# Performance work log

Measured on AMD Instinct MI355X. Metric: run time of the kernel, lower is better.

Reference implementation:

```python
import jax, jax.numpy as jnp
import numpy as np
from jax import lax

NUM_CLASSES = 80
SCALE_XY = 1.0
NMS_THRESH = 0.7
SCORE_THRESH = 0.05
OBJ_THRESH = 0.5
MAX_DETS = 100  # fixed top-K candidate pool fed to NMS (jit-friendly padding)


def setup_inputs() -> dict:
    key = jax.random.key(0)
    k1, k2 = jax.random.split(key)
    x = jax.random.normal(k1, (16, 255, 128, 128), dtype=jnp.float32)
    anchors = jax.random.uniform(k2, (3, 2), dtype=jnp.float32, minval=0.05, maxval=0.7)
    return {"x": x, "anchors": anchors}


def decode(x, anchors):
    # x: [b, A*(5+C), h, w] -> boxes [b,h,w,A,4], obj [b,h,w,A], scores [b,h,w,A,C]
    b, _, h, w = x.shape
    A = anchors.shape[0]
    out = x.reshape(b, A, 5 + NUM_CLASSES, h, w).transpose(0, 3, 4, 1, 2)
    c_x = jnp.arange(w, dtype=jnp.float32).reshape(1, 1, w, 1)
    c_y = jnp.arange(h, dtype=jnp.float32).reshape(1, h, 1, 1)
    b_xy = SCALE_XY * jax.nn.sigmoid(out[..., :2]) - 0.5 * (SCALE_XY - 1.0)
    b_x = (b_xy[..., 0] + c_x) / w
    b_y = (b_xy[..., 1] + c_y) / h
    b_wh = jnp.clip(jnp.exp(out[..., 2:4]) * anchors.reshape(1, 1, 1, A, 2), 0.0, 2.0)
    top_left = jnp.stack([b_x, b_y], axis=-1) - 0.5 * b_wh
    boxes = jnp.concatenate([top_left, top_left + b_wh], axis=-1)
    return boxes, out[..., 4], out[..., 5:]


def box_iou(a, b):
    # a: [N,4], b: [M,4] in (x1,y1,x2,y2)
    area_a = jnp.clip(a[:, 2] - a[:, 0], 0) * jnp.clip(a[:, 3] - a[:, 1], 0)
    area_b = jnp.clip(b[:, 2] - b[:, 0], 0) * jnp.clip(b[:, 3] - b[:, 1], 0)
    lt = jnp.maximum(a[:, None, :2], b[None, :, :2])
    rb = jnp.minimum(a[:, None, 2:], b[None, :, 2:])
    wh = jnp.clip(rb - lt, 0)
    inter = wh[..., 0] * wh[..., 1]
    union = area_a[:, None] + area_b[None, :] - inter
    return inter / jnp.maximum(union, 1e-12)


def greedy_nms(iou, valid):
    # boxes assumed sorted by descending score; valid: [K] bool
    K = iou.shape[0]
    idx = jnp.arange(K)

    def body(i, keep):
        # if box i is kept, suppress later boxes overlapping it too much
        sup = keep[i] & (iou[i] > NMS_THRESH) & (idx > i)
        return keep & ~sup

    return lax.fori_loop(0, K, body, valid)


def _per_image(boxes, b_o, b_scores):
    # boxes [h,w,A,4], b_o [h,w,A], b_scores [h,w,A,C]
    boxes = jnp.clip(boxes.reshape(-1, 4), 0.0, 1.0)
    obj = jax.nn.sigmoid(b_o.reshape(-1))
    cls = jax.nn.sigmoid(b_scores.reshape(-1, NUM_CLASSES))
    cls_score = cls.max(axis=-1)
    labels = jnp.argmax(cls, axis=-1)
    scores = cls_score * obj
    valid = (obj >= OBJ_THRESH) & (scores >= SCORE_THRESH)
    masked = jnp.where(valid, scores, -1.0)
    top_s, top_i = lax.top_k(masked, MAX_DETS)
    top_boxes = boxes[top_i]
    top_labels = labels[top_i]
    cand = top_s > 0.0
    keep = greedy_nms(box_iou(top_boxes, top_boxes), cand)
    out_boxes = jnp.where(keep[:, None], top_boxes, 0.0)
    out_scores = jnp.where(keep, top_s, 0.0)
    out_labels = jnp.where(keep, top_labels, -1)
    return out_boxes, out_scores, out_labels, keep


def reference(x, anchors):
    boxes, b_o, b_scores = decode(x, anchors)
    # fixed-size padded detections per image (equivalent to post_process with
    # dynamic lists, padded to MAX_DETS; keep mask marks valid rows)
    return jax.vmap(_per_image)(boxes, b_o, b_scores)
```

## Files before the change

### kernel.cpp

```cpp
#include <hip/hip_runtime.h>
#include <math.h>

#define B 16
#define A 3
#define W 128
#define HW 16384
#define NCH 255
#define NCLS 80
#define NCAND 49152
#define K 100
#define NBINS 4096
#define CAP 1024

__device__ __forceinline__ float sigmoidf_(float v) {
    return 1.0f / (1.0f + expf(-v));
}

__device__ __forceinline__ bool pair_before(float sa, int ia, float sb, int ib) {
    return (sa > sb) || (sa == sb && ia < ib);
}

__global__ __launch_bounds__(256) void k_scores(const float* __restrict__ x,
                                                float* __restrict__ scores,
                                                unsigned char* __restrict__ labels) {
    int tid = blockIdx.x * 256 + threadIdx.x;
    int g = tid & 3;
    int grp = tid >> 2;
    int b = grp / (A * HW / 4);
    int r = grp - b * (A * HW / 4);
    int a = r / (HW / 4);
    int q = r - a * (HW / 4);
    int hw = q * 4;
    const float* base = x + (size_t)(b * NCH + a * 85) * HW + hw;

    float4 o4 = make_float4(0.f, 0.f, 0.f, 0.f);
    if (g == 0) o4 = *(const float4*)(base + 4 * HW);

    int c0 = g * 20;
    float4 m4 = *(const float4*)(base + (size_t)(5 + c0) * HW);
    int amx = c0, amy = c0, amz = c0, amw = c0;
    #pragma unroll
    for (int k = 1; k < 20; ++k) {
        int c = c0 + k;
        float4 v = *(const float4*)(base + (size_t)(5 + c) * HW);
        bool gx = v.x > m4.x; amx = gx ? c : amx; m4.x = gx ? v.x : m4.x;
        bool gy = v.y > m4.y; amy = gy ? c : amy; m4.y = gy ? v.y : m4.y;
        bool gz = v.z > m4.z; amz = gz ? c : amz; m4.z = gz ? v.z : m4.z;
        bool gw = v.w > m4.w; amw = gw ? c : amw; m4.w = gw ? v.w : m4.w;
    }
    #pragma unroll
    for (int d = 1; d <= 2; d <<= 1) {
        float vx = __shfl_xor(m4.x, d); int jx = __shfl_xor(amx, d);
        float vy = __shfl_xor(m4.y, d); int jy = __shfl_xor(amy, d);
        float vz = __shfl_xor(m4.z, d); int jz = __shfl_xor(amz, d);
        float vw = __shfl_xor(m4.w, d); int jw = __shfl_xor(amw, d);
        if (vx > m4.x || (vx == m4.x && jx < amx)) { m4.x = vx; amx = jx; }
        if (vy > m4.y || (vy == m4.y && jy < amy)) { m4.y = vy; amy = jy; }
        if (vz > m4.z || (vz == m4.z && jz < amz)) { m4.z = vz; amz = jz; }
        if (vw > m4.w || (vw == m4.w && jw < amw)) { m4.w = vw; amw = jw; }
    }

    if (g == 0) {
        float ol[4] = {o4.x, o4.y, o4.z, o4.w};
        float ml[4] = {m4.x, m4.y, m4.z, m4.w};
        float outv[4];
        #pragma unroll
        for (int l = 0; l < 4; ++l) {
            float obj = sigmoidf_(ol[l]);
            float cls = sigmoidf_(ml[l]);
            float sc = obj * cls;
            bool valid = (obj >= 0.5f) && (sc >= 0.05f);
            outv[l] = valid ? sc : -1.0f;
        }
        size_t off = (size_t)b * NCAND + a * HW + hw;
        *(float4*)(scores + off) = make_float4(outv[0], outv[1], outv[2], outv[3]);
        *(uchar4*)(labels + off) = make_uchar4((unsigned char)amx, (unsigned char)amy,
                                               (unsigned char)amz, (unsigned char)amw);
    }
}

__global__ __launch_bounds__(1024) void k_tail(const float* __restrict__ x,
                                               const float* __restrict__ anchors,
                                               const float* __restrict__ scores,
                                               const unsigned char* __restrict__ labels,
                                               float* __restrict__ out) {
    __shared__ unsigned int lh[NBINS];
    __shared__ int sh_thr;
    __shared__ unsigned int sh_cnt;
    __shared__ float cs[CAP];
    __shared__ int ci[CAP];
    __shared__ float ts[K];
    __shared__ int tix[K];
    __shared__ float bx[K][4];
    __shared__ float area[K];
    __shared__ int lab[K];
    __shared__ unsigned int sup[K][4];
    __shared__ unsigned int keepw[4];

    int b = blockIdx.x;
    int tid = threadIdx.x;
    const float* sb = scores + (size_t)b * NCAND;

    for (int i = tid; i < NBINS; i += 1024) lh[i] = 0;
    if (tid == 0) { sh_thr = 0; sh_cnt = 0; }
    if (tid < 4) keepw[tid] = 0u;
    for (int i = tid; i < K * 4; i += 1024) ((unsigned int*)sup)[i] = 0u;
    if (tid < K) { ts[tid] = -3.0f; tix[tid] = 0x7FFFFFFF; }
    __syncthreads();

    #pragma unroll
    for (int it = 0; it < 12; ++it) {
        int o = (it * 1024 + tid) * 4;
        float4 v = *(const float4*)(sb + o);
        float sv[4] = {v.x, v.y, v.z, v.w};
        #pragma unroll
        for (int l = 0; l < 4; ++l) {
            float s = sv[l];
            if (s > 0.0f) {
                int bin = (int)(s * (float)NBINS);
                bin = bin > NBINS - 1 ? NBINS - 1 : bin;
                atomicAdd(&lh[bin], 1u);
            }
        }
    }
    __syncthreads();

    if (tid < 64) {
        unsigned int c = 0;
        #pragma unroll
        for (int j = 0; j < 64; ++j)
            c += lh[tid * 64 + ((j + tid) & 63)];
        unsigned int s = c;
        #pragma unroll
        for (int off = 1; off < 64; off <<= 1) {
            unsigned int v = __shfl_down(s, off);
            if (tid + off < 64) s += v;
        }
        unsigned long long mask = __ballot(s >= K);
        int lstar = -1;
        if (mask) lstar = 63 - __clzll(mask);
        unsigned int snext = 0;
        if (lstar >= 0 && lstar < 63) snext = (unsigned int)__shfl((int)s, lstar + 1);
        if (lstar >= 0 && tid == lstar) {
            unsigned int running = snext;
            int result = lstar * 64;
            for (int bin = lstar * 64 + 63; bin >= lstar * 64; --bin) {
                running += lh[bin];
                if (running >= K) { result = bin; break; }
            }
            sh_thr = result;
        }
    }
    __syncthreads();

    int thr = sh_thr;
    #pragma unroll
    for (int it = 0; it < 12; ++it) {
        int o = (it * 1024 + tid) * 4;
        float4 v = *(const float4*)(sb + o);
        float sv[4] = {v.x, v.y, v.z, v.w};
        #pragma unroll
        for (int l = 0; l < 4; ++l) {
            float s = sv[l];
            if (s > 0.0f && (int)(s * (float)NBINS) >= thr) {
                unsigned int p = atomicAdd(&sh_cnt, 1u);
                if (p < CAP) {
                    int so = o + l;
                    int aa = so >> 14;
                    int hh = so & (HW - 1);
                    cs[p] = s;
                    ci[p] = hh * A + aa;
                }
            }
        }
    }
    __syncthreads();
    int n = (int)sh_cnt; if (n > CAP) n = CAP;

    if (tid < n) {
        float s0 = cs[tid]; int i0 = ci[tid];
        int rank = 0;
        for (int j = 0; j < n; ++j)
            rank += pair_before(cs[j], ci[j], s0, i0) ? 1 : 0;
        if (rank < K) { ts[rank] = s0; tix[rank] = i0; }
    }
    __syncthreads();

    if (tid < K && ts[tid] > 0.0f) {
        int nidx = tix[tid];
        int a = nidx % A;
        int hw = nidx / A;
        int cx = hw % W;
        int cy = hw / W;
        const float* base = x + (size_t)(b * NCH + a * 85) * HW + hw;
        float tx = base[0];
        float ty = base[HW];
        float tw = base[2 * HW];
        float th = base[3 * HW];
        float bcx = (sigmoidf_(tx) + (float)cx) / 128.0f;
        float bcy = (sigmoidf_(ty) + (float)cy) / 128.0f;
        float bw = fminf(fmaxf(expf(tw) * anchors[a * 2 + 0], 0.0f), 2.0f);
        float bh = fminf(fmaxf(expf(th) * anchors[a * 2 + 1], 0.0f), 2.0f);
        float x1 = bcx - 0.5f * bw;
        float y1 = bcy - 0.5f * bh;
        float x2 = x1 + bw;
        float y2 = y1 + bh;
        x1 = fminf(fmaxf(x1, 0.0f), 1.0f);
        y1 = fminf(fmaxf(y1, 0.0f), 1.0f);
        x2 = fminf(fmaxf(x2, 0.0f), 1.0f);
        y2 = fminf(fmaxf(y2, 0.0f), 1.0f);
        bx[tid][0] = x1; bx[tid][1] = y1; bx[tid][2] = x2; bx[tid][3] = y2;
        area[tid] = fmaxf(x2 - x1, 0.0f) * fmaxf(y2 - y1, 0.0f);
        lab[tid] = (int)labels[(size_t)b * NCAND + a * HW + hw];
        atomicOr(&keepw[tid >> 5], 1u << (tid & 31));
    }
    __syncthreads();

    for (int p = tid; p < K * K; p += 1024) {
        int i = p / K, j = p % K;
        if (j > i && ts[i] > 0.0f && ts[j] > 0.0f) {
            float lx = fmaxf(bx[i][0], bx[j][0]);
            float ly = fmaxf(bx[i][1], bx[j][1]);
            float rx = fminf(bx[i][2], bx[j][2]);
            float ry = fminf(bx[i][3], bx[j][3]);
            float iw = fmaxf(rx - lx, 0.0f);
            float ih = fmaxf(ry - ly, 0.0f);
            float inter = iw * ih;
            float uni = area[i] + area[j] - inter;
            float iou = inter / fmaxf(uni, 1e-12f);
            if (iou > 0.7f) atomicOr(&sup[i][j >> 5], 1u << (j & 31));
        }
    }
    __syncthreads();

    if (tid == 0) {
        unsigned int kw0 = keepw[0], kw1 = keepw[1], kw2 = keepw[2], kw3 = keepw[3];
        for (int i = 0; i < K; ++i) {
            unsigned int kwi = (i < 32) ? kw0 : (i < 64) ? kw1 : (i < 96) ? kw2 : kw3;
            if ((kwi >> (i & 31)) & 1u) {
                kw0 &= ~sup[i][0];
                kw1 &= ~sup[i][1];
                kw2 &= ~sup[i][2];
                kw3 &= ~sup[i][3];
            }
        }
        keepw[0] = kw0; keepw[1] = kw1; keepw[2] = kw2; keepw[3] = kw3;
    }
    __syncthreads();

    if (tid < K) {
        int kp = (keepw[tid >> 5] >> (tid & 31)) & 1u;
        float sc = ts[tid];
        float* ob = out + (size_t)b * K * 4;
        float* osc = out + (size_t)B * K * 4;
        float* olab = osc + (size_t)B * K;
        float* okp = olab + (size_t)B * K;
        ob[tid * 4 + 0] = kp ? bx[tid][0] : 0.0f;
        ob[tid * 4 + 1] = kp ? bx[tid][1] : 0.0f;
        ob[tid * 4 + 2] = kp ? bx[tid][2] : 0.0f;
        ob[tid * 4 + 3] = kp ? bx[tid][3] : 0.0f;
        osc[b * K + tid] = kp ? sc : 0.0f;
        olab[b * K + tid] = kp ? (float)lab[tid] : -1.0f;
        okp[b * K + tid] = kp ? 1.0f : 0.0f;
    }
}

extern "C" void kernel_launch(void* const* d_in, const int* in_sizes, int n_in,
                              void* d_out, int out_size, void* d_ws, size_t ws_size,
                              hipStream_t stream) {
    const float* x = (const float*)d_in[0];
    const float* anchors = (const float*)d_in[1];
    float* out = (float*)d_out;

    float* scores = (float*)d_ws;
    unsigned char* labels = (unsigned char*)(scores + (size_t)B * NCAND);

    k_scores<<<(B * A * HW) / 256, 256, 0, stream>>>(x, scores, labels);
    k_tail<<<B, 1024, 0, stream>>>(x, anchors, scores, labels, out);
}
```

Baseline: 72.94 us.

## Fuse score pass and per-image tail into one kernel via last-block counter

Merges the class max/argmax scoring kernel and the per-image top-K/NMS tail into one kernel. Each image gets 12 blocks of 1024 threads, and each thread now scans all 80 classes for 4 pixels instead of splitting the classes over 4 threads. A per-image atomic counter, zeroed by a small extra kernel, lets the last finishing block run the selection and NMS. This removes the dependency gap between the two launches. In exchange the grid shrinks to 192 blocks with fewer threads per pixel, which may cut the loads in flight on a bandwidth-bound read.

```diff
diff --git a/kernel.cpp b/kernel.cpp
--- a/kernel.cpp
+++ b/kernel.cpp
@@ -11,6 +11,7 @@
 #define K 100
 #define NBINS 4096
 #define CAP 1024
+#define BLKS_PER_IMG 12
 
 __device__ __forceinline__ float sigmoidf_(float v) {
     return 1.0f / (1.0f + expf(-v));
@@ -20,70 +21,16 @@
     return (sa > sb) || (sa == sb && ia < ib);
 }
 
-__global__ __launch_bounds__(256) void k_scores(const float* __restrict__ x,
-                                                float* __restrict__ scores,
-                                                unsigned char* __restrict__ labels) {
-    int tid = blockIdx.x * 256 + threadIdx.x;
-    int g = tid & 3;
-    int grp = tid >> 2;
-    int b = grp / (A * HW / 4);
-    int r = grp - b * (A * HW / 4);
-    int a = r / (HW / 4);
-    int q = r - a * (HW / 4);
-    int hw = q * 4;
-    const float* base = x + (size_t)(b * NCH + a * 85) * HW + hw;
-
-    float4 o4 = make_float4(0.f, 0.f, 0.f, 0.f);
-    if (g == 0) o4 = *(const float4*)(base + 4 * HW);
-
-    int c0 = g * 20;
-    float4 m4 = *(const float4*)(base + (size_t)(5 + c0) * HW);
-    int amx = c0, amy = c0, amz = c0, amw = c0;
-    #pragma unroll
-    for (int k = 1; k < 20; ++k) {
-        int c = c0 + k;
-        float4 v = *(const float4*)(base + (size_t)(5 + c) * HW);
-        bool gx = v.x > m4.x; amx = gx ? c : amx; m4.x = gx ? v.x : m4.x;
-        bool gy = v.y > m4.y; amy = gy ? c : amy; m4.y = gy ? v.y : m4.y;
-        bool gz = v.z > m4.z; amz = gz ? c : amz; m4.z = gz ? v.z : m4.z;
-        bool gw = v.w > m4.w; amw = gw ? c : amw; m4.w = gw ? v.w : m4.w;
-    }
-    #pragma unroll
-    for (int d = 1; d <= 2; d <<= 1) {
-        float vx = __shfl_xor(m4.x, d); int jx = __shfl_xor(amx, d);
-        float vy = __shfl_xor(m4.y, d); int jy = __shfl_xor(amy, d);
-        float vz = __shfl_xor(m4.z, d); int jz = __shfl_xor(amz, d);
-        float vw = __shfl_xor(m4.w, d); int jw = __shfl_xor(amw, d);
-        if (vx > m4.x || (vx == m4.x && jx < amx)) { m4.x = vx; amx = jx; }
-        if (vy > m4.y || (vy == m4.y && jy < amy)) { m4.y = vy; amy = jy; }
-        if (vz > m4.z || (vz == m4.z && jz < amz)) { m4.z = vz; amz = jz; }
-        if (vw > m4.w || (vw == m4.w && jw < amw)) { m4.w = vw; amw = jw; }
-    }
-
-    if (g == 0) {
-        float ol[4] = {o4.x, o4.y, o4.z, o4.w};
-        float ml[4] = {m4.x, m4.y, m4.z, m4.w};
-        float outv[4];
-        #pragma unroll
-        for (int l = 0; l < 4; ++l) {
-            float obj = sigmoidf_(ol[l]);
-            float cls = sigmoidf_(ml[l]);
-            float sc = obj * cls;
-            bool valid = (obj >= 0.5f) && (sc >= 0.05f);
-            outv[l] = valid ? sc : -1.0f;
-        }
-        size_t off = (size_t)b * NCAND + a * HW + hw;
-        *(float4*)(scores + off) = make_float4(outv[0], outv[1], outv[2], outv[3]);
-        *(uchar4*)(labels + off) = make_uchar4((unsigned char)amx, (unsigned char)amy,
-                                               (unsigned char)amz, (unsigned char)amw);
-    }
-}
-
-__global__ __launch_bounds__(1024) void k_tail(const float* __restrict__ x,
-                                               const float* __restrict__ anchors,
-                                               const float* __restrict__ scores,
-                                               const unsigned char* __restrict__ labels,
-                                               float* __restrict__ out) {
+__global__ __launch_bounds__(64) void k_zero(unsigned int* __restrict__ done) {
+    if (threadIdx.x < B) done[threadIdx.x] = 0u;
+}
+
+__global__ __launch_bounds__(1024, 8) void k_fused(const float* __restrict__ x,
+                                                   const float* __restrict__ anchors,
+                                                   float* __restrict__ scores,
+                                                   unsigned char* __restrict__ labels,
+                                                   unsigned int* __restrict__ done,
+                                                   float* __restrict__ out) {
     __shared__ unsigned int lh[NBINS];
     __shared__ int sh_thr;
     __shared__ unsigned int sh_cnt;
@@ -91,14 +38,62 @@
     __shared__ int ci[CAP];
     __shared__ float ts[K];
     __shared__ int tix[K];
-    __shared__ float bx[K][4];
+    __shared__ float bxs[K][4];
     __shared__ float area[K];
     __shared__ int lab[K];
     __shared__ unsigned int sup[K][4];
     __shared__ unsigned int keepw[4];
-
-    int b = blockIdx.x;
+    __shared__ int lastf;
+
+    int bid = blockIdx.x;
+    int b = bid / BLKS_PER_IMG;
+    int seg = bid % BLKS_PER_IMG;
     int tid = threadIdx.x;
+
+    {
+        int off = seg * 4096 + tid * 4;
+        int a = off >> 14;
+        int hw = off & (HW - 1);
+        const float* base = x + (size_t)(b * NCH + a * 85) * HW + hw;
+
+        float4 o4 = *(const float4*)(base + 4 * HW);
+        float4 m4 = *(const float4*)(base + 5 * HW);
+        int amx = 0, amy = 0, amz = 0, amw = 0;
+        #pragma unroll
+        for (int c = 1; c < NCLS; ++c) {
+            float4 v = *(const float4*)(base + (size_t)(5 + c) * HW);
+            bool gx = v.x > m4.x; amx = gx ? c : amx; m4.x = gx ? v.x : m4.x;
+            bool gy = v.y > m4.y; amy = gy ? c : amy; m4.y = gy ? v.y : m4.y;
+            bool gz = v.z > m4.z; amz = gz ? c : amz; m4.z = gz ? v.z : m4.z;
+            bool gw = v.w > m4.w; amw = gw ? c : amw; m4.w = gw ? v.w : m4.w;
+        }
+        float ol[4] = {o4.x, o4.y, o4.z, o4.w};
+        float ml[4] = {m4.x, m4.y, m4.z, m4.w};
+        float outv[4];
+        #pragma unroll
+        for (int l = 0; l < 4; ++l) {
+            float obj = sigmoidf_(ol[l]);
+            float cls = sigmoidf_(ml[l]);
+            float sc = obj * cls;
+            bool valid = (obj >= 0.5f) && (sc >= 0.05f);
+            outv[l] = valid ? sc : -1.0f;
+        }
+        size_t soff = (size_t)b * NCAND + off;
+        *(float4*)(scores + soff) = make_float4(outv[0], outv[1], outv[2], outv[3]);
+        *(uchar4*)(labels + soff) = make_uchar4((unsigned char)amx, (unsigned char)amy,
+                                                (unsigned char)amz, (unsigned char)amw);
+    }
+
+    __threadfence();
+    __syncthreads();
+    if (tid == 0) {
+        unsigned int old = atomicAdd(&done[b], 1u);
+        lastf = (old == BLKS_PER_IMG - 1) ? 1 : 0;
+    }
+    __syncthreads();
+    if (!lastf) return;
+    __threadfence();
+
     const float* sb = scores + (size_t)b * NCAND;
 
     for (int i = tid; i < NBINS; i += 1024) lh[i] = 0;
@@ -209,7 +204,7 @@
         y1 = fminf(fmaxf(y1, 0.0f), 1.0f);
         x2 = fminf(fmaxf(x2, 0.0f), 1.0f);
         y2 = fminf(fmaxf(y2, 0.0f), 1.0f);
-        bx[tid][0] = x1; bx[tid][1] = y1; bx[tid][2] = x2; bx[tid][3] = y2;
+        bxs[tid][0] = x1; bxs[tid][1] = y1; bxs[tid][2] = x2; bxs[tid][3] = y2;
         area[tid] = fmaxf(x2 - x1, 0.0f) * fmaxf(y2 - y1, 0.0f);
         lab[tid] = (int)labels[(size_t)b * NCAND + a * HW + hw];
         atomicOr(&keepw[tid >> 5], 1u << (tid & 31));
@@ -219,10 +214,10 @@
     for (int p = tid; p < K * K; p += 1024) {
         int i = p / K, j = p % K;
         if (j > i && ts[i] > 0.0f && ts[j] > 0.0f) {
-            float lx = fmaxf(bx[i][0], bx[j][0]);
-            float ly = fmaxf(bx[i][1], bx[j][1]);
-            float rx = fminf(bx[i][2], bx[j][2]);
-            float ry = fminf(bx[i][3], bx[j][3]);
+            float lx = fmaxf(bxs[i][0], bxs[j][0]);
+            float ly = fmaxf(bxs[i][1], bxs[j][1]);
+            float rx = fminf(bxs[i][2], bxs[j][2]);
+            float ry = fminf(bxs[i][3], bxs[j][3]);
             float iw = fmaxf(rx - lx, 0.0f);
             float ih = fmaxf(ry - ly, 0.0f);
             float inter = iw * ih;
@@ -255,10 +250,10 @@
         float* osc = out + (size_t)B * K * 4;
         float* olab = osc + (size_t)B * K;
         float* okp = olab + (size_t)B * K;
-        ob[tid * 4 + 0] = kp ? bx[tid][0] : 0.0f;
-        ob[tid * 4 + 1] = kp ? bx[tid][1] : 0.0f;
-        ob[tid * 4 + 2] = kp ? bx[tid][2] : 0.0f;
-        ob[tid * 4 + 3] = kp ? bx[tid][3] : 0.0f;
+        ob[tid * 4 + 0] = kp ? bxs[tid][0] : 0.0f;
+        ob[tid * 4 + 1] = kp ? bxs[tid][1] : 0.0f;
+        ob[tid * 4 + 2] = kp ? bxs[tid][2] : 0.0f;
+        ob[tid * 4 + 3] = kp ? bxs[tid][3] : 0.0f;
         osc[b * K + tid] = kp ? sc : 0.0f;
         olab[b * K + tid] = kp ? (float)lab[tid] : -1.0f;
         okp[b * K + tid] = kp ? 1.0f : 0.0f;
@@ -274,7 +269,8 @@
 
     float* scores = (float*)d_ws;
     unsigned char* labels = (unsigned char*)(scores + (size_t)B * NCAND);
-
-    k_scores<<<(B * A * HW) / 256, 256, 0, stream>>>(x, scores, labels);
-    k_tail<<<B, 1024, 0, stream>>>(x, anchors, scores, labels, out);
-}
+    unsigned int* done = (unsigned int*)(labels + (size_t)B * NCAND);
+
+    k_zero<<<1, 64, 0, stream>>>(done);
+    k_fused<<<B * BLKS_PER_IMG, 1024, 0, stream>>>(x, anchors, scores, labels, done, out);
+}
```

After: 180.9 us. 2.48x slower.

## Assign one thread per 4 pixels over all classes with nontemporal loads

Applied to the files above, without the earlier changes.

The score kernel no longer splits the 80-class argmax across 4 lanes with shuffle reductions. Each thread now scans all 80 class channels for 4 pixels, and the grid shrinks by a factor of 4. Loads switch to nontemporal builtins to avoid polluting cache with streamed input. This removes the shuffles and the idle lanes during the epilogue, but each thread has a longer serial load chain and there are fewer threads to hide memory latency.

```diff
diff --git a/kernel.cpp b/kernel.cpp
--- a/kernel.cpp
+++ b/kernel.cpp
@@ -12,71 +12,57 @@
 #define NBINS 4096
 #define CAP 1024
 
+typedef float floatx4 __attribute__((ext_vector_type(4)));
+
 __device__ __forceinline__ float sigmoidf_(float v) {
     return 1.0f / (1.0f + expf(-v));
 }
 
 __device__ __forceinline__ bool pair_before(float sa, int ia, float sb, int ib) {
     return (sa > sb) || (sa == sb && ia < ib);
+}
+
+__device__ __forceinline__ floatx4 nt_load4(const float* p) {
+    return __builtin_nontemporal_load((const floatx4*)p);
 }
 
 __global__ __launch_bounds__(256) void k_scores(const float* __restrict__ x,
                                                 float* __restrict__ scores,
                                                 unsigned char* __restrict__ labels) {
-    int tid = blockIdx.x * 256 + threadIdx.x;
-    int g = tid & 3;
-    int grp = tid >> 2;
-    int b = grp / (A * HW / 4);
-    int r = grp - b * (A * HW / 4);
+    int t = blockIdx.x * 256 + threadIdx.x;
+    int b = t / (A * HW / 4);
+    int r = t - b * (A * HW / 4);
     int a = r / (HW / 4);
     int q = r - a * (HW / 4);
     int hw = q * 4;
     const float* base = x + (size_t)(b * NCH + a * 85) * HW + hw;
 
-    float4 o4 = make_float4(0.f, 0.f, 0.f, 0.f);
-    if (g == 0) o4 = *(const float4*)(base + 4 * HW);
-
-    int c0 = g * 20;
-    float4 m4 = *(const float4*)(base + (size_t)(5 + c0) * HW);
-    int amx = c0, amy = c0, amz = c0, amw = c0;
-    #pragma unroll
-    for (int k = 1; k < 20; ++k) {
-        int c = c0 + k;
-        float4 v = *(const float4*)(base + (size_t)(5 + c) * HW);
+    floatx4 o4 = nt_load4(base + 4 * HW);
+    floatx4 m4 = nt_load4(base + 5 * HW);
+    int amx = 0, amy = 0, amz = 0, amw = 0;
+    #pragma unroll
+    for (int c = 1; c < NCLS; ++c) {
+        floatx4 v = nt_load4(base + (size_t)(5 + c) * HW);
         bool gx = v.x > m4.x; amx = gx ? c : amx; m4.x = gx ? v.x : m4.x;
         bool gy = v.y > m4.y; amy = gy ? c : amy; m4.y = gy ? v.y : m4.y;
         bool gz = v.z > m4.z; amz = gz ? c : amz; m4.z = gz ? v.z : m4.z;
         bool gw = v.w > m4.w; amw = gw ? c : amw; m4.w = gw ? v.w : m4.w;
     }
-    #pragma unroll
-    for (int d = 1; d <= 2; d <<= 1) {
-        float vx = __shfl_xor(m4.x, d); int jx = __shfl_xor(amx, d);
-        float vy = __shfl_xor(m4.y, d); int jy = __shfl_xor(amy, d);
-        float vz = __shfl_xor(m4.z, d); int jz = __shfl_xor(amz, d);
-        float vw = __shfl_xor(m4.w, d); int jw = __shfl_xor(amw, d);
-        if (vx > m4.x || (vx == m4.x && jx < amx)) { m4.x = vx; amx = jx; }
-        if (vy > m4.y || (vy == m4.y && jy < amy)) { m4.y = vy; amy = jy; }
-        if (vz > m4.z || (vz == m4.z && jz < amz)) { m4.z = vz; amz = jz; }
-        if (vw > m4.w || (vw == m4.w && jw < amw)) { m4.w = vw; amw = jw; }
-    }
-
-    if (g == 0) {
-        float ol[4] = {o4.x, o4.y, o4.z, o4.w};
-        float ml[4] = {m4.x, m4.y, m4.z, m4.w};
-        float outv[4];
-        #pragma unroll
-        for (int l = 0; l < 4; ++l) {
-            float obj = sigmoidf_(ol[l]);
-            float cls = sigmoidf_(ml[l]);
-            float sc = obj * cls;
-            bool valid = (obj >= 0.5f) && (sc >= 0.05f);
-            outv[l] = valid ? sc : -1.0f;
-        }
-        size_t off = (size_t)b * NCAND + a * HW + hw;
-        *(float4*)(scores + off) = make_float4(outv[0], outv[1], outv[2], outv[3]);
-        *(uchar4*)(labels + off) = make_uchar4((unsigned char)amx, (unsigned char)amy,
-                                               (unsigned char)amz, (unsigned char)amw);
-    }
+    float ol[4] = {o4.x, o4.y, o4.z, o4.w};
+    float ml[4] = {m4.x, m4.y, m4.z, m4.w};
+    float outv[4];
+    #pragma unroll
+    for (int l = 0; l < 4; ++l) {
+        float obj = sigmoidf_(ol[l]);
+        float cls = sigmoidf_(ml[l]);
+        float sc = obj * cls;
+        bool valid = (obj >= 0.5f) && (sc >= 0.05f);
+        outv[l] = valid ? sc : -1.0f;
+    }
+    size_t off = (size_t)b * NCAND + a * HW + hw;
+    *(float4*)(scores + off) = make_float4(outv[0], outv[1], outv[2], outv[3]);
+    *(uchar4*)(labels + off) = make_uchar4((unsigned char)amx, (unsigned char)amy,
+                                           (unsigned char)amz, (unsigned char)amw);
 }
 
 __global__ __launch_bounds__(1024) void k_tail(const float* __restrict__ x,
@@ -275,6 +261,6 @@
     float* scores = (float*)d_ws;
     unsigned char* labels = (unsigned char*)(scores + (size_t)B * NCAND);
 
-    k_scores<<<(B * A * HW) / 256, 256, 0, stream>>>(x, scores, labels);
+    k_scores<<<(B * A * HW / 4) / 256, 256, 0, stream>>>(x, scores, labels);
     k_tail<<<B, 1024, 0, stream>>>(x, anchors, scores, labels, out);
 }
```

Result: slower. 93.61 us (+28.3%).
